# Performance work log

Hardware: AMD Instinct MI355X
Metric: run time of the kernel (lower is better)

The kernel has to match this reference:

```python
import jax, jax.numpy as jnp
import numpy as np

N = 50000      # nodes
E = 800000     # edges
D = 256        # num_feat == num_hidden == out_dim
G = 64         # graphs in batch
C = 64         # num_classes
L = 2          # cells (layers)
S = 2          # GNN steps per cell
SCALE = 0.05


def setup_inputs() -> dict:
    key = jax.random.key(0)
    ks = jax.random.split(key, 10)
    x = jax.random.normal(ks[0], (N, D), jnp.float32)
    edge_index = jax.random.randint(ks[1], (2, E), 0, N, dtype=jnp.int64)
    edge_attr = jax.random.normal(ks[2], (E, 1), jnp.float32)
    batch = jnp.sort(jax.random.randint(ks[3], (N,), 0, G, dtype=jnp.int64))
    pre_w = jax.random.normal(ks[4], (L, 2, D, D), jnp.float32) * SCALE
    pre_b = jax.random.normal(ks[5], (L, 2, D), jnp.float32) * SCALE
    gcn_w = jax.random.normal(ks[6], (L, S, D, D), jnp.float32) * SCALE
    gcn_b = jax.random.normal(ks[7], (L, S, D), jnp.float32) * SCALE
    cls_w = jax.random.normal(ks[8], (D, C), jnp.float32) * SCALE
    cls_b = jax.random.normal(ks[9], (C,), jnp.float32) * SCALE
    return {"x": x, "edge_index": edge_index, "edge_attr": edge_attr,
            "batch": batch, "pre_w": pre_w, "pre_b": pre_b,
            "gcn_w": gcn_w, "gcn_b": gcn_b, "cls_w": cls_w, "cls_b": cls_b}


def reference(x, edge_index, edge_attr, batch, pre_w, pre_b, gcn_w, gcn_b, cls_w, cls_b):
    n = x.shape[0]
    # GCNConv with self-loops and symmetric normalization (torch_geometric default)
    loops = jnp.arange(n, dtype=edge_index.dtype)
    src = jnp.concatenate([edge_index[0], loops])   # [E+N]
    dst = jnp.concatenate([edge_index[1], loops])   # [E+N]
    deg = jax.ops.segment_sum(jnp.ones_like(dst, dtype=x.dtype), dst, num_segments=n)
    dinv = jax.lax.rsqrt(deg)                        # deg >= 1 due to self loops
    norm = (dinv[src] * dinv[dst])[:, None]          # [E+N, 1]

    def gcn(h, w, b):
        hw = h @ w                                   # [N, D]
        msg = hw[src] * norm                         # gather + scale
        return jax.ops.segment_sum(msg, dst, num_segments=n) + b

    def cell(s0, s1, l):
        s0 = s0 @ pre_w[l, 0] + pre_b[l, 0]
        s1 = s1 @ pre_w[l, 1] + pre_b[l, 1]
        states = [s0, s1]
        for i, idx in enumerate((0, 1)):             # NAS indices [0, 1]
            states.append(gcn(states[idx], gcn_w[l, i], gcn_b[l, i]))
        # concat='add': tmp = states[2]; then accumulate states[2:] again
        tmp = states[2]
        for st in states[2:]:
            tmp = tmp + st                           # = 2*s2 + s3 (faithful)
        return tmp

    s0 = s1 = x
    for l in range(L):
        s0, s1 = s1, cell(s0, s1, l)
    out = s1                                         # [N, D]

    g = cls_b.shape[0] if False else G
    counts = jax.ops.segment_sum(jnp.ones((n,), x.dtype), batch, num_segments=G)
    mean_pool = jax.ops.segment_sum(out, batch, num_segments=G) / jnp.maximum(counts, 1.0)[:, None]
    max_pool = jax.ops.segment_max(out, batch, num_segments=G)
    max_pool = jnp.where(counts[:, None] > 0, max_pool, 0.0)
    pooled = mean_pool + max_pool                    # [G, D]
    return pooled @ cls_w + cls_b                    # [G, C]
```

## Files before the change

### kernel.cpp

```cpp
#include <hip/hip_runtime.h>

typedef __attribute__((ext_vector_type(8))) short bf16x8;
typedef __attribute__((ext_vector_type(4))) float f32x4;

__device__ inline float bf2f(unsigned short u) {
    union { float f; unsigned int i; } v; v.i = ((unsigned int)u) << 16; return v.f;
}
__device__ inline unsigned short f2bf(float f) {
    union { float f; unsigned int u; } v; v.f = f;
    unsigned int x = v.u;
    unsigned int r = x + 0x7FFFu + ((x >> 16) & 1u);
    return (unsigned short)(r >> 16);
}
__device__ inline unsigned int fenc(float x) {
    union { float f; unsigned int u; } v; v.f = x;
    return (v.u & 0x80000000u) ? ~v.u : (v.u | 0x80000000u);
}
__device__ inline float fdec(unsigned int k) {
    union { float f; unsigned int u; } v;
    v.u = (k & 0x80000000u) ? (k & 0x7FFFFFFFu) : ~k;
    return v.f;
}
__device__ inline float ldf(const void* p, size_t i, int f32) {
    return f32 ? ((const float*)p)[i] : bf2f(((const unsigned short*)p)[i]);
}
__device__ inline int ldi(const int* p, size_t i, int i64) {
    return i64 ? p[2 * i] : p[i];
}

__global__ __launch_bounds__(256)
void k_detect(const unsigned short* __restrict__ xu, int xstride,
              const int* __restrict__ ei, int estride, int* __restrict__ flags) {
    __shared__ int cnt, orv;
    if (threadIdx.x == 0) { cnt = 0; orv = 0; }
    __syncthreads();
    int c = 0, o = 0;
    for (int s = 0; s < 4; ++s) {
        int j = threadIdx.x * 4 + s;
        size_t k = (size_t)j * xstride;
        unsigned short u = xu[2 * k];
        int e = (u >> 7) & 0xFF;
        if (e >= 100 && e <= 140) ++c;
        size_t idx = (size_t)j * estride;
        o |= ei[2 * idx + 1];
    }
    atomicAdd(&cnt, c); atomicOr(&orv, o);
    __syncthreads();
    if (threadIdx.x == 0) {
        flags[0] = (cnt < 768) ? 1 : 0;
        flags[1] = (orv == 0) ? 1 : 0;
    }
}

__global__ void k_zero(int* __restrict__ hist, int* __restrict__ cursor,
                       float* __restrict__ psum, unsigned int* __restrict__ pkey,
                       int* __restrict__ pcnt, int N) {
    int t = blockIdx.x * 256 + threadIdx.x;
    if (t < N) hist[t] = 0;
    else if (t < 2 * N) cursor[t - N] = 0;
    else if (t < 2 * N + 16384) psum[t - 2 * N] = 0.f;
    else if (t < 2 * N + 32768) pkey[t - 2 * N - 16384] = 0u;
    else if (t < 2 * N + 32768 + 64) pcnt[t - 2 * N - 32768] = 0;
}

__global__ __launch_bounds__(256)
void k_cvt(const void* __restrict__ X, unsigned short* __restrict__ Xb,
           size_t nelem, const int* __restrict__ flags) {
    int f = flags[0];
    size_t i = ((size_t)blockIdx.x * 256 + threadIdx.x) * 8;
    if (i >= nelem) return;
    if (f) {
        const float* s = (const float*)X + i;
        float4 f0 = *(const float4*)s;
        float4 f1 = *(const float4*)(s + 4);
        int4 o;
        o.x = (int)f2bf(f0.x) | ((int)f2bf(f0.y) << 16);
        o.y = (int)f2bf(f0.z) | ((int)f2bf(f0.w) << 16);
        o.z = (int)f2bf(f1.x) | ((int)f2bf(f1.y) << 16);
        o.w = (int)f2bf(f1.z) | ((int)f2bf(f1.w) << 16);
        *(int4*)(Xb + i) = o;
    } else {
        *(int4*)(Xb + i) = *(const int4*)((const unsigned short*)X + i);
    }
}

__global__ __launch_bounds__(256)
void k_cvtw(const void* __restrict__ pre_w, const void* __restrict__ gcn_w,
            unsigned short* __restrict__ Pb, unsigned short* __restrict__ Gt,
            const int* __restrict__ flags) {
    __shared__ float tile[64][65];
    const int i = blockIdx.y;
    const int m0 = (blockIdx.x & 3) * 64;
    const int n0 = (blockIdx.x >> 2) * 64;
    const int f = flags[0];
    const size_t base = (size_t)i * 65536;
#pragma unroll
    for (int q = 0; q < 16; ++q) {
        int idx = q * 256 + threadIdx.x;
        int r = idx >> 6, c = idx & 63;
        size_t src = base + (size_t)(m0 + r) * 256 + n0 + c;
        Pb[src] = f2bf(ldf(pre_w, src, f));
        tile[r][c] = ldf(gcn_w, src, f);
    }
    __syncthreads();
#pragma unroll
    for (int q = 0; q < 16; ++q) {
        int idx = q * 256 + threadIdx.x;
        int r = idx >> 6, c = idx & 63;
        Gt[base + (size_t)(n0 + r) * 256 + m0 + c] = f2bf(tile[c][r]);
    }
}

__global__ __launch_bounds__(256)
void k_prepw(const unsigned short* __restrict__ Pb, const unsigned short* __restrict__ Gt,
             unsigned short* __restrict__ Wt0, unsigned short* __restrict__ Wt1) {
    const int which = blockIdx.y;
    const int wid = threadIdx.x >> 6, lane = threadIdx.x & 63;
    const int tile = blockIdx.x * 4 + wid;
    const int n0 = (tile >> 4) * 16, k0 = (tile & 15) * 16;
    const int l15 = lane & 15, hi = lane >> 4;
    size_t base0, base1 = 0;
    if (which == 0)      { base0 = 0; base1 = 65536; }
    else if (which == 1) { base0 = 2 * 65536; }
    else                 { base0 = 3 * 65536; }
    f32x4 acc0 = {}, acc1 = {};
    const unsigned short* ga = Gt + base0 + (size_t)(n0 + l15) * 256 + hi * 8;
    const unsigned short* pa = Pb + base0 + (size_t)(k0 + l15) * 256 + hi * 8;
    const unsigned short* gb = Gt + base1 + (size_t)(n0 + l15) * 256 + hi * 8;
    const unsigned short* pb = Pb + base1 + (size_t)(k0 + l15) * 256 + hi * 8;
#pragma unroll
    for (int kt = 0; kt < 8; ++kt) {
        bf16x8 a0 = *(const bf16x8*)(ga + kt * 32);
        bf16x8 b0 = *(const bf16x8*)(pa + kt * 32);
        acc0 = __builtin_amdgcn_mfma_f32_16x16x32_bf16(a0, b0, acc0, 0, 0, 0);
        if (which == 0) {
            bf16x8 a1 = *(const bf16x8*)(gb + kt * 32);
            bf16x8 b1 = *(const bf16x8*)(pb + kt * 32);
            acc1 = __builtin_amdgcn_mfma_f32_16x16x32_bf16(a1, b1, acc1, 0, 0, 0);
        }
    }
#pragma unroll
    for (int j = 0; j < 4; ++j) {
        int n = n0 + hi * 4 + j;
        int k = k0 + l15;
        if (which == 0)      Wt0[(size_t)n * 256 + k]       = f2bf(2.f * acc0[j] + acc1[j]);
        else if (which == 1) Wt1[(size_t)n * 512 + k]       = f2bf(2.f * acc0[j]);
        else                 Wt1[(size_t)n * 512 + 256 + k] = f2bf(acc0[j]);
    }
}

__global__ __launch_bounds__(256)
void k_prepb(const void* __restrict__ pre_b, const unsigned short* __restrict__ Gt,
             const void* __restrict__ gcn_b,
             float* __restrict__ cvec, float* __restrict__ dvec,
             const int* __restrict__ flags) {
    __shared__ float pb[2][256];
    const int l = blockIdx.x, n = threadIdx.x;
    const int f = flags[0];
    pb[0][n] = ldf(pre_b, (size_t)(l * 2 + 0) * 256 + n, f);
    pb[1][n] = ldf(pre_b, (size_t)(l * 2 + 1) * 256 + n, f);
    __syncthreads();
    const unsigned short* g0 = Gt + (size_t)(l * 2 + 0) * 65536 + (size_t)n * 256;
    const unsigned short* g1 = Gt + (size_t)(l * 2 + 1) * 65536 + (size_t)n * 256;
    float a = 0.f, b = 0.f;
#pragma unroll 4
    for (int mc = 0; mc < 32; ++mc) {
        bf16x8 v0 = *(const bf16x8*)(g0 + mc * 8);
        bf16x8 v1 = *(const bf16x8*)(g1 + mc * 8);
#pragma unroll
        for (int u = 0; u < 8; ++u) {
            a += pb[0][mc * 8 + u] * bf2f((unsigned short)v0[u]);
            b += pb[1][mc * 8 + u] * bf2f((unsigned short)v1[u]);
        }
    }
    cvec[l * 256 + n] = 2.f * a + b;
    dvec[l * 256 + n] = 2.f * ldf(gcn_b, (size_t)(l * 2 + 0) * 256 + n, f)
                            + ldf(gcn_b, (size_t)(l * 2 + 1) * 256 + n, f);
}

__global__ void k_hist(const int* __restrict__ ei, int E, int N,
                       int* __restrict__ hist, const int* __restrict__ flags) {
    int e = blockIdx.x * 256 + threadIdx.x;
    if (e >= E) return;
    int i64 = flags[1];
    int d = ldi(ei, (size_t)E + e, i64); d = d < 0 ? 0 : (d >= N ? N - 1 : d);
    atomicAdd(&hist[d], 1);
}

__global__ __launch_bounds__(256)
void k_scan1(const int* __restrict__ hist, int* __restrict__ pre,
             int* __restrict__ bsum, int N) {
    __shared__ int s[256];
    int i = blockIdx.x * 256 + threadIdx.x;
    int v = (i < N) ? hist[i] : 0;
    s[threadIdx.x] = v;
    __syncthreads();
    for (int off = 1; off < 256; off <<= 1) {
        int t = (threadIdx.x >= off) ? s[threadIdx.x - off] : 0;
        __syncthreads();
        s[threadIdx.x] += t;
        __syncthreads();
    }
    if (i < N) pre[i] = s[threadIdx.x] - v;
    if (threadIdx.x == 255) bsum[blockIdx.x] = s[255];
}

__global__ __launch_bounds__(256)
void k_scan2(const int* __restrict__ bsum, int* __restrict__ boff,
             int* __restrict__ rowptr, int nb, int N) {
    __shared__ int s[256];
    int t = threadIdx.x;
    int v = (t < nb) ? bsum[t] : 0;
    s[t] = v;
    __syncthreads();
    for (int off = 1; off < 256; off <<= 1) {
        int x = (t >= off) ? s[t - off] : 0;
        __syncthreads();
        s[t] += x;
        __syncthreads();
    }
    if (t < nb) boff[t] = s[t] - v;
    if (t == nb - 1) rowptr[N] = s[t];
}

__global__ __launch_bounds__(256)
void k_scan3(const int* __restrict__ hist, const int* __restrict__ pre,
             const int* __restrict__ boff, int* __restrict__ rowptr,
             float* __restrict__ dinv, int N) {
    int i = blockIdx.x * 256 + threadIdx.x;
    if (i < N) {
        rowptr[i] = pre[i] + boff[blockIdx.x];
        dinv[i] = rsqrtf((float)(hist[i] + 1));
    }
}

__global__ void k_scatter(const int* __restrict__ ei, int E, int N,
                          const int* __restrict__ rowptr, int* __restrict__ cursor,
                          int* __restrict__ col, const int* __restrict__ flags) {
    int e = blockIdx.x * 256 + threadIdx.x;
    if (e >= E) return;
    int i64 = flags[1];
    int s = ldi(ei, (size_t)e, i64);     s = s < 0 ? 0 : (s >= N ? N - 1 : s);
    int d = ldi(ei, (size_t)E + e, i64); d = d < 0 ? 0 : (d >= N ? N - 1 : d);
    int pos = rowptr[d] + atomicAdd(&cursor[d], 1);
    col[pos] = s;
}

__global__ __launch_bounds__(256)
void k_gemm(const unsigned short* __restrict__ Xb, const unsigned short* __restrict__ Yb,
            const unsigned short* __restrict__ Wt, const float* __restrict__ cvec,
            const float* __restrict__ dinv, unsigned short* __restrict__ out,
            int M, int K) {
    __shared__ unsigned short lds[2 * 128 * 64];
    char* ldsb = (char*)lds;
    const int tid = threadIdx.x;
    const int lane = tid & 63;
    const int wid = tid >> 6;
    const int wm = wid >> 1, wn = wid & 1;
    const int row0 = blockIdx.x * 128;
    const int bn = blockIdx.y;

    f32x4 acc[4][4] = {};
    const int KT = K / 64;
    for (int kt = 0; kt < KT; ++kt) {
        const int k0 = kt * 64;
        const unsigned short* Asrc = (k0 < 256) ? Xb : Yb;
        const int ak0 = (k0 < 256) ? k0 : k0 - 256;
        int4 ra[4], rw[4];
#pragma unroll
        for (int q = 0; q < 4; ++q) {
            int id = q * 256 + tid;
            int r = id >> 3;
            int cb = id & 7;
            int grow = row0 + r; if (grow > M - 1) grow = M - 1;
            ra[q] = *(const int4*)(Asrc + (size_t)grow * 256 + ak0 + cb * 8);
            rw[q] = *(const int4*)(Wt + (size_t)(bn * 128 + r) * K + k0 + cb * 8);
        }
        __syncthreads();
#pragma unroll
        for (int q = 0; q < 4; ++q) {
            int id = q * 256 + tid;
            int r = id >> 3, cb = id & 7;
            int sw = (cb * 16) ^ ((r & 7) << 4);
            *(int4*)(ldsb + r * 128 + sw) = ra[q];
            *(int4*)(ldsb + 16384 + r * 128 + sw) = rw[q];
        }
        __syncthreads();
#pragma unroll
        for (int kk = 0; kk < 2; ++kk) {
            bf16x8 af[4], bfr[4];
            int byte = kk * 64 + ((lane >> 4) << 4);
#pragma unroll
            for (int m = 0; m < 4; ++m) {
                int r = wm * 64 + m * 16 + (lane & 15);
                af[m] = *(const bf16x8*)(ldsb + r * 128 + (byte ^ ((r & 7) << 4)));
            }
#pragma unroll
            for (int n = 0; n < 4; ++n) {
                int r = wn * 64 + n * 16 + (lane & 15);
                bfr[n] = *(const bf16x8*)(ldsb + 16384 + r * 128 + (byte ^ ((r & 7) << 4)));
            }
#pragma unroll
            for (int m = 0; m < 4; ++m)
#pragma unroll
                for (int n = 0; n < 4; ++n)
                    acc[m][n] = __builtin_amdgcn_mfma_f32_16x16x32_bf16(af[m], bfr[n], acc[m][n], 0, 0, 0);
        }
    }
#pragma unroll
    for (int m = 0; m < 4; ++m) {
#pragma unroll
        for (int j = 0; j < 4; ++j) {
            int rt = wm * 64 + m * 16 + ((lane >> 4) << 2) + j;
            int grow = row0 + rt;
            if (grow < M) {
                float di = dinv[grow];
#pragma unroll
                for (int n = 0; n < 4; ++n) {
                    int colc = bn * 128 + wn * 64 + n * 16 + (lane & 15);
                    float v = (acc[m][n][j] + cvec[colc]) * di;
                    out[(size_t)grow * 256 + colc] = f2bf(v);
                }
            }
        }
    }
}

__global__ __launch_bounds__(256)
void k_agg(const unsigned short* __restrict__ U, const int* __restrict__ rowptr,
           const int* __restrict__ col, const float* __restrict__ dinv,
           const float* __restrict__ dvec, unsigned short* __restrict__ Y, int N) {
    int w = (blockIdx.x * 256 + threadIdx.x) >> 6;
    int lane = threadIdx.x & 63;
    if (w >= N) return;
    const size_t loff = (size_t)lane * 4;
    ushort4 sv = *(const ushort4*)(U + (size_t)w * 256 + loff);
    float a0 = bf2f(sv.x), a1 = bf2f(sv.y), a2 = bf2f(sv.z), a3 = bf2f(sv.w);
    int beg = rowptr[w], end = rowptr[w + 1];
    int e = beg;
    for (; e + 16 <= end; e += 16) {
        int s[16];
        ushort4 v[16];
#pragma unroll
        for (int u = 0; u < 16; ++u) s[u] = __builtin_amdgcn_readfirstlane(col[e + u]);
#pragma unroll
        for (int u = 0; u < 16; ++u) v[u] = *(const ushort4*)(U + (size_t)s[u] * 256 + loff);
#pragma unroll
        for (int u = 0; u < 16; ++u) {
            a0 += bf2f(v[u].x); a1 += bf2f(v[u].y);
            a2 += bf2f(v[u].z); a3 += bf2f(v[u].w);
        }
    }
    for (; e + 4 <= end; e += 4) {
        int s[4];
        ushort4 v[4];
#pragma unroll
        for (int u = 0; u < 4; ++u) s[u] = __builtin_amdgcn_readfirstlane(col[e + u]);
#pragma unroll
        for (int u = 0; u < 4; ++u) v[u] = *(const ushort4*)(U + (size_t)s[u] * 256 + loff);
#pragma unroll
        for (int u = 0; u < 4; ++u) {
            a0 += bf2f(v[u].x); a1 += bf2f(v[u].y);
            a2 += bf2f(v[u].z); a3 += bf2f(v[u].w);
        }
    }
    for (; e < end; ++e) {
        int s = __builtin_amdgcn_readfirstlane(col[e]);
        ushort4 v = *(const ushort4*)(U + (size_t)s * 256 + loff);
        a0 += bf2f(v.x); a1 += bf2f(v.y); a2 += bf2f(v.z); a3 += bf2f(v.w);
    }
    float di = dinv[w];
    int f = lane * 4;
    a0 = a0 * di + dvec[f + 0];
    a1 = a1 * di + dvec[f + 1];
    a2 = a2 * di + dvec[f + 2];
    a3 = a3 * di + dvec[f + 3];
    ushort4 o; o.x = f2bf(a0); o.y = f2bf(a1); o.z = f2bf(a2); o.w = f2bf(a3);
    *(ushort4*)(Y + (size_t)w * 256 + loff) = o;
}

__global__ __launch_bounds__(256)
void k_pool(const unsigned short* __restrict__ Y, const int* __restrict__ batch, int N,
            float* __restrict__ psum, unsigned int* __restrict__ pkey, int* __restrict__ pcnt,
            const int* __restrict__ flags) {
    int f = threadIdx.x;
    int base = blockIdx.x * 64;
    if (base >= N) return;
    int i64 = flags[1];
    int g0 = ldi(batch, base, i64); int curg = g0 < 0 ? 0 : (g0 > 63 ? 63 : g0);
    float s = 0.f, mx = -__builtin_inff(); int cnt = 0;
#pragma unroll 4
    for (int r = 0; r < 64; ++r) {
        int node = base + r;
        if (node >= N) break;
        int g = ldi(batch, node, i64); g = g < 0 ? 0 : (g > 63 ? 63 : g);
        if (g != curg) {
            atomicAdd(&psum[curg * 256 + f], s);
            atomicMax(&pkey[curg * 256 + f], fenc(mx));
            if (f == 0) atomicAdd(&pcnt[curg], cnt);
            curg = g; s = 0.f; mx = -__builtin_inff(); cnt = 0;
        }
        float v = bf2f(Y[(size_t)node * 256 + f]);
        s += v; mx = fmaxf(mx, v); ++cnt;
    }
    atomicAdd(&psum[curg * 256 + f], s);
    atomicMax(&pkey[curg * 256 + f], fenc(mx));
    if (f == 0) atomicAdd(&pcnt[curg], cnt);
}

__global__ __launch_bounds__(64)
void k_cls(const float* __restrict__ psum, const unsigned int* __restrict__ pkey,
           const int* __restrict__ pcnt, const void* __restrict__ clsw,
           const void* __restrict__ clsb, float* __restrict__ outf,
           unsigned short* __restrict__ outu, const int* __restrict__ flags) {
    __shared__ float pooled[256];
    int g = blockIdx.x, c = threadIdx.x;
    int f = flags[0];
    int cnt = pcnt[g];
    for (int m = c; m < 256; m += 64) {
        float mean = psum[g * 256 + m] / (float)(cnt > 0 ? cnt : 1);
        float mx = (cnt > 0) ? fdec(pkey[g * 256 + m]) : 0.f;
        pooled[m] = mean + mx;
    }
    __syncthreads();
    float a = ldf(clsb, c, f);
#pragma unroll 8
    for (int m = 0; m < 256; ++m) a += pooled[m] * ldf(clsw, (size_t)m * 64 + c, f);
    if (f) outf[g * 64 + c] = a;
    else   outu[g * 64 + c] = f2bf(a);
}

extern "C" void kernel_launch(void* const* d_in, const int* in_sizes, int n_in,
                              void* d_out, int out_size, void* d_ws, size_t ws_size,
                              hipStream_t stream) {
    const void*           X     = d_in[0];
    const int*            EI    = (const int*)d_in[1];
    const int*            BATCH = (const int*)d_in[3];
    const void*           PREW  = d_in[4];
    const void*           PREB  = d_in[5];
    const void*           GCNW  = d_in[6];
    const void*           GCNB  = d_in[7];
    const void*           CLSW  = d_in[8];
    const void*           CLSB  = d_in[9];

    const int N = in_sizes[3];
    const int E = in_sizes[1] / 2;
    const int NB = (N + 255) / 256;

    char* ws = (char*)d_ws;
    size_t off = 0;
    auto alloc = [&](size_t b) { size_t o = off; off += (b + 255) & ~(size_t)255; return o; };
    int*            flags  = (int*)(ws + alloc(256));
    float*          dinv   = (float*)(ws + alloc((size_t)N * 4));
    int*            hist   = (int*)(ws + alloc((size_t)N * 4));
    int*            cursor = (int*)(ws + alloc((size_t)N * 4));
    int*            rowptr = (int*)(ws + alloc((size_t)(N + 1) * 4));
    int*            pre    = (int*)(ws + alloc((size_t)N * 4));
    int*            bsum   = (int*)(ws + alloc((size_t)NB * 4));
    int*            boff   = (int*)(ws + alloc((size_t)NB * 4));
    int*            col    = (int*)(ws + alloc((size_t)E * 4));
    unsigned short* Pb     = (unsigned short*)(ws + alloc(4 * 65536 * 2));
    unsigned short* Gt     = (unsigned short*)(ws + alloc(4 * 65536 * 2));
    unsigned short* Wt0    = (unsigned short*)(ws + alloc(256 * 256 * 2));
    unsigned short* Wt1    = (unsigned short*)(ws + alloc(256 * 512 * 2));
    float*          cvec   = (float*)(ws + alloc(512 * 4));
    float*          dvec   = (float*)(ws + alloc(512 * 4));
    float*          psum   = (float*)(ws + alloc(64 * 256 * 4));
    unsigned int*   pkey   = (unsigned int*)(ws + alloc(64 * 256 * 4));
    int*            pcnt   = (int*)(ws + alloc(64 * 4));
    unsigned short* Xb     = (unsigned short*)(ws + alloc((size_t)N * 256 * 2));
    unsigned short* U      = (unsigned short*)(ws + alloc((size_t)N * 256 * 2));
    unsigned short* Y      = (unsigned short*)(ws + alloc((size_t)N * 256 * 2));

    int zt = 2 * N + 32768 + 64;
    k_zero<<<(zt + 255) / 256, 256, 0, stream>>>(hist, cursor, psum, pkey, pcnt, N);

    int xstride = (in_sizes[0] / 2) / 1024; if (xstride < 1) xstride = 1;
    int estride = E / 1024;                 if (estride < 1) estride = 1;
    k_detect<<<1, 256, 0, stream>>>((const unsigned short*)X, xstride, EI, estride, flags);

    size_t xelem = (size_t)N * 256;
    k_cvt<<<(int)((xelem / 8 + 255) / 256), 256, 0, stream>>>(X, Xb, xelem, flags);

    k_hist<<<(E + 255) / 256, 256, 0, stream>>>(EI, E, N, hist, flags);
    k_scan1<<<NB, 256, 0, stream>>>(hist, pre, bsum, N);
    k_scan2<<<1, 256, 0, stream>>>(bsum, boff, rowptr, NB, N);
    k_scan3<<<NB, 256, 0, stream>>>(hist, pre, boff, rowptr, dinv, N);
    k_scatter<<<(E + 255) / 256, 256, 0, stream>>>(EI, E, N, rowptr, cursor, col, flags);

    k_cvtw<<<dim3(16, 4), 256, 0, stream>>>(PREW, GCNW, Pb, Gt, flags);
    k_prepw<<<dim3(64, 3), 256, 0, stream>>>(Pb, Gt, Wt0, Wt1);
    k_prepb<<<2, 256, 0, stream>>>(PREB, Gt, GCNB, cvec, dvec, flags);

    dim3 ggrid((N + 127) / 128, 2);
    k_gemm<<<ggrid, 256, 0, stream>>>(Xb, U, Wt0, cvec, dinv, U, N, 256);
    k_agg<<<(N + 3) / 4, 256, 0, stream>>>(U, rowptr, col, dinv, dvec, Y, N);
    k_gemm<<<ggrid, 256, 0, stream>>>(Xb, Y, Wt1, cvec + 256, dinv, U, N, 512);
    k_agg<<<(N + 3) / 4, 256, 0, stream>>>(U, rowptr, col, dinv, dvec + 256, Y, N);
    k_pool<<<(N + 63) / 64, 256, 0, stream>>>(Y, BATCH, N, psum, pkey, pcnt, flags);
    k_cls<<<64, 64, 0, stream>>>(psum, pkey, pcnt, CLSW, CLSB,
                                 (float*)d_out, (unsigned short*)d_out, flags);
}
```

Baseline: 430.3 us.

## Compute full 256-wide output per GEMM block and stage epilogue through LDS

Each GEMM block now covers all 256 output columns with 512 threads (8 waves) rather than splitting N across two blocks. The A tile is therefore loaded from global memory once instead of twice. The epilogue writes bf16 results into LDS and then stores coalesced 16-byte rows to global, replacing scattered 2-byte stores. In exchange, LDS use rises to 48KB per block, which may lower occupancy, and the grid has half as many blocks.

After: 403.5 us. -6.2%, faster.

```diff
diff --git a/kernel.cpp b/kernel.cpp
--- a/kernel.cpp
+++ b/kernel.cpp
@@ -246,19 +246,18 @@
     col[pos] = s;
 }
 
-__global__ __launch_bounds__(256)
+__global__ __launch_bounds__(512)
 void k_gemm(const unsigned short* __restrict__ Xb, const unsigned short* __restrict__ Yb,
             const unsigned short* __restrict__ Wt, const float* __restrict__ cvec,
             const float* __restrict__ dinv, unsigned short* __restrict__ out,
             int M, int K) {
-    __shared__ unsigned short lds[2 * 128 * 64];
-    char* ldsb = (char*)lds;
+    __shared__ char ldsb[49152];
     const int tid = threadIdx.x;
     const int lane = tid & 63;
     const int wid = tid >> 6;
-    const int wm = wid >> 1, wn = wid & 1;
+    const int wm = wid >> 2, wn = wid & 3;
+    const int l15 = lane & 15, hi = lane >> 4;
     const int row0 = blockIdx.x * 128;
-    const int bn = blockIdx.y;
 
     f32x4 acc[4][4] = {};
     const int KT = K / 64;
@@ -266,38 +265,48 @@
         const int k0 = kt * 64;
         const unsigned short* Asrc = (k0 < 256) ? Xb : Yb;
         const int ak0 = (k0 < 256) ? k0 : k0 - 256;
-        int4 ra[4], rw[4];
-#pragma unroll
-        for (int q = 0; q < 4; ++q) {
-            int id = q * 256 + tid;
-            int r = id >> 3;
-            int cb = id & 7;
+        int4 ra[2], rw[4];
+#pragma unroll
+        for (int q = 0; q < 2; ++q) {
+            int id = q * 512 + tid;
+            int r = id >> 3, cb = id & 7;
             int grow = row0 + r; if (grow > M - 1) grow = M - 1;
             ra[q] = *(const int4*)(Asrc + (size_t)grow * 256 + ak0 + cb * 8);
-            rw[q] = *(const int4*)(Wt + (size_t)(bn * 128 + r) * K + k0 + cb * 8);
-        }
-        __syncthreads();
+        }
 #pragma unroll
         for (int q = 0; q < 4; ++q) {
-            int id = q * 256 + tid;
+            int id = q * 512 + tid;
+            int r = id >> 3, cb = id & 7;
+            rw[q] = *(const int4*)(Wt + (size_t)r * K + k0 + cb * 8);
+        }
+        __syncthreads();
+#pragma unroll
+        for (int q = 0; q < 2; ++q) {
+            int id = q * 512 + tid;
             int r = id >> 3, cb = id & 7;
             int sw = (cb * 16) ^ ((r & 7) << 4);
             *(int4*)(ldsb + r * 128 + sw) = ra[q];
+        }
+#pragma unroll
+        for (int q = 0; q < 4; ++q) {
+            int id = q * 512 + tid;
+            int r = id >> 3, cb = id & 7;
+            int sw = (cb * 16) ^ ((r & 7) << 4);
             *(int4*)(ldsb + 16384 + r * 128 + sw) = rw[q];
         }
         __syncthreads();
 #pragma unroll
         for (int kk = 0; kk < 2; ++kk) {
             bf16x8 af[4], bfr[4];
-            int byte = kk * 64 + ((lane >> 4) << 4);
+            int byte = kk * 64 + (hi << 4);
 #pragma unroll
             for (int m = 0; m < 4; ++m) {
-                int r = wm * 64 + m * 16 + (lane & 15);
+                int r = wm * 64 + m * 16 + l15;
                 af[m] = *(const bf16x8*)(ldsb + r * 128 + (byte ^ ((r & 7) << 4)));
             }
 #pragma unroll
             for (int n = 0; n < 4; ++n) {
-                int r = wn * 64 + n * 16 + (lane & 15);
+                int r = wn * 64 + n * 16 + l15;
                 bfr[n] = *(const bf16x8*)(ldsb + 16384 + r * 128 + (byte ^ ((r & 7) << 4)));
             }
 #pragma unroll
@@ -307,21 +316,35 @@
                     acc[m][n] = __builtin_amdgcn_mfma_f32_16x16x32_bf16(af[m], bfr[n], acc[m][n], 0, 0, 0);
         }
     }
-#pragma unroll
-    for (int m = 0; m < 4; ++m) {
-#pragma unroll
-        for (int j = 0; j < 4; ++j) {
-            int rt = wm * 64 + m * 16 + ((lane >> 4) << 2) + j;
-            int grow = row0 + rt;
-            if (grow < M) {
-                float di = dinv[grow];
-#pragma unroll
-                for (int n = 0; n < 4; ++n) {
-                    int colc = bn * 128 + wn * 64 + n * 16 + (lane & 15);
-                    float v = (acc[m][n][j] + cvec[colc]) * di;
-                    out[(size_t)grow * 256 + colc] = f2bf(v);
+    for (int half = 0; half < 2; ++half) {
+        __syncthreads();
+        if (wm == half) {
+#pragma unroll
+            for (int m = 0; m < 4; ++m) {
+#pragma unroll
+                for (int j = 0; j < 4; ++j) {
+                    int rl = m * 16 + hi * 4 + j;
+                    int grow = row0 + half * 64 + rl;
+                    if (grow < M) {
+                        float di = dinv[grow];
+#pragma unroll
+                        for (int n = 0; n < 4; ++n) {
+                            int colc = wn * 64 + n * 16 + l15;
+                            float v = (acc[m][n][j] + cvec[colc]) * di;
+                            *(unsigned short*)(ldsb + rl * 512 + colc * 2) = f2bf(v);
+                        }
+                    }
                 }
             }
+        }
+        __syncthreads();
+#pragma unroll
+        for (int p = 0; p < 4; ++p) {
+            int rl = p * 16 + (tid >> 5);
+            int cb = tid & 31;
+            int grow = row0 + half * 64 + rl;
+            if (grow < M)
+                *(int4*)(out + (size_t)grow * 256 + cb * 8) = *(const int4*)(ldsb + rl * 512 + cb * 16);
         }
     }
 }
@@ -492,10 +515,10 @@
     k_prepw<<<dim3(64, 3), 256, 0, stream>>>(Pb, Gt, Wt0, Wt1);
     k_prepb<<<2, 256, 0, stream>>>(PREB, Gt, GCNB, cvec, dvec, flags);
 
-    dim3 ggrid((N + 127) / 128, 2);
-    k_gemm<<<ggrid, 256, 0, stream>>>(Xb, U, Wt0, cvec, dinv, U, N, 256);
+    int ggrid = (N + 127) / 128;
+    k_gemm<<<ggrid, 512, 0, stream>>>(Xb, U, Wt0, cvec, dinv, U, N, 256);
     k_agg<<<(N + 3) / 4, 256, 0, stream>>>(U, rowptr, col, dinv, dvec, Y, N);
-    k_gemm<<<ggrid, 256, 0, stream>>>(Xb, Y, Wt1, cvec + 256, dinv, U, N, 512);
+    k_gemm<<<ggrid, 512, 0, stream>>>(Xb, Y, Wt1, cvec + 256, dinv, U, N, 512);
     k_agg<<<(N + 3) / 4, 256, 0, stream>>>(U, rowptr, col, dinv, dvec + 256, Y, N);
     k_pool<<<(N + 63) / 64, 256, 0, stream>>>(Y, BATCH, N, psum, pkey, pcnt, flags);
     k_cls<<<64, 64, 0, stream>>>(psum, pkey, pcnt, CLSW, CLSB,
```
